# Kernel tuning notes

Measured on AMD Instinct MI355X. Metric: run time of the kernel, lower is better.

## Reference

```python
import jax, jax.numpy as jnp
import numpy as np

CH = 128
KSIZE = 7
BS, H, W = 8, 56, 56


def nbhd_extract(x, k):
    """Faithful replication of square_nbhd_extractor(k)(x) from the torch code,
    including its permute(0,2,1).reshape(bs,h,w,d) layout reinterpretation and
    the unfold over the last two dims of that layout. x: (bs, n, d) -> (bs, n, k*k, d)."""
    bs, n, d = x.shape
    h = w = int(np.sqrt(n))
    # torch: x.permute(0,2,1).reshape(bs,h,w,d)
    y = jnp.transpose(x, (0, 2, 1)).reshape(bs, h, w, d)
    # extract_image_patches treats y as (b, c=h, H=w, W=d); stride=1, dilation=1
    # pad both sliding dims by k-1 total ((k-1)//2 low, rest high)
    p_lo = (k - 1) // 2
    p_hi = (k - 1) - p_lo
    yp = jnp.pad(y, ((0, 0), (0, 0), (p_lo, p_hi), (p_lo, p_hi)))
    Hs, Ws = w, d  # output sliding sizes equal original dims (stride 1)
    # double unfold: window over dim2 at axis -2, window over dim3 at axis -1
    wins = jnp.stack([
        jnp.stack([yp[:, :, i:i + Hs, j:j + Ws] for j in range(k)], axis=-1)
        for i in range(k)], axis=-2)  # (bs, h, w, d, k, k)
    patches = jnp.transpose(wins, (0, 4, 5, 1, 2, 3))  # (bs, k, k, h, w, d)
    # torch: patches.view(bs, n, d, r).permute(0,1,3,2)
    return patches.reshape(bs, n, d, k * k).transpose(0, 1, 3, 2)  # (bs, n, r, d)


def setup_inputs() -> dict:
    key = jax.random.key(0)
    ks = jax.random.split(key, 3)
    x = jax.random.normal(ks[0], (BS, CH, H, W), dtype=jnp.float32)
    W1 = jax.random.normal(ks[1], (2, CH), dtype=jnp.float32) * np.float32(1.0 / np.sqrt(2.0))
    b1 = jnp.zeros((CH,), dtype=jnp.float32)
    W2 = jax.random.normal(ks[2], (CH, CH), dtype=jnp.float32) * np.float32(1.0 / np.sqrt(CH))
    b2 = jnp.zeros((CH,), dtype=jnp.float32)
    return {"x": x, "W1": W1, "b1": b1, "W2": W2, "b2": b2, "ksize": KSIZE}


def reference(x, W1, b1, W2, b2, ksize):
    bs, c, h, w = x.shape
    n = h * w
    # coords: meshgrid('ij') of linspace(-3,3), shape (1, n, 2)
    gi = jnp.linspace(-3.0, 3.0, h)
    gj = jnp.linspace(-3.0, 3.0, w)
    coords = jnp.stack(jnp.meshgrid(gi, gj, indexing='ij'), axis=-1).reshape(1, n, 2)
    rel = nbhd_extract(coords, ksize) - coords[:, :, None, :]  # (1, n, r, 2)
    # position MLP: Linear(2,ch) -> ReLU -> Linear(ch,ch)
    P = jax.nn.relu(rel @ W1 + b1) @ W2 + b2                   # (1, n, r, ch)
    Wsm = jax.nn.softmax(P, axis=2)[0]                          # (n, r, c) ; ch == c
    # values: gather neighborhood patches of channels-last points
    xp = jnp.transpose(x, (0, 2, 3, 1)).reshape(bs, n, c)
    V = nbhd_extract(xp, ksize)                                 # (bs, n, r, c)
    # head-folded weighting * value reduce over neighborhood == per-channel weighted sum
    out = jnp.einsum('nrc,bnrc->bnc', Wsm, V)                   # (bs, n, c)
    return jnp.transpose(out, (0, 2, 1)).reshape(bs, c, h, w)
```

## Files before the change

kernel.cpp:

```cpp
#include <hip/hip_runtime.h>

#define CH   128
#define KS   7
#define R    49
#define HH   56
#define NPOS 3136
#define BS   8
#define XSTR 401408
#define XTOT (BS*XSTR)

typedef short short8 __attribute__((ext_vector_type(8)));
typedef float f32x4  __attribute__((ext_vector_type(4)));
typedef unsigned int u32;
typedef unsigned long long u64;
typedef u32 u32x4 __attribute__((ext_vector_type(4)));

__device__ __forceinline__ short f2bf(float f) {
    unsigned u = __float_as_uint(f);
    u += 0x7fffu + ((u >> 16) & 1u);
    return (short)(u >> 16);
}
__device__ __forceinline__ float bf2f(short s) {
    return __uint_as_float(((unsigned)(unsigned short)s) << 16);
}
__device__ __forceinline__ float bf2f_u(u32 lo16) {
    return __uint_as_float(lo16 << 16);
}
__device__ __forceinline__ u64 bitrange(int a, int b) {
    a = a < 0 ? 0 : (a > 49 ? 49 : a);
    b = b < 0 ? 0 : (b > 49 ? 49 : b);
    if (b <= a) return 0ull;
    return (1ull << b) - (1ull << a);
}

#define HSTR 136
#define PSTR 132
#define NWIN 3140

__global__ __launch_bounds__(256) void poatt_prep(
    const float* __restrict__ W2, short* __restrict__ wsH, short* __restrict__ wsL)
{
    int t = blockIdx.x * 256 + threadIdx.x;
    int k = t >> 7, ch = t & 127;
    float w = W2[k * CH + ch];
    short hi = f2bf(w);
    wsH[ch * CH + k] = hi;
    wsL[ch * CH + k] = f2bf(w - bf2f(hi));
}

__global__ __launch_bounds__(256) void poatt_pc(
    const float* __restrict__ x, const float* __restrict__ W2,
    u32* __restrict__ x2, short* __restrict__ wsH, short* __restrict__ wsL)
{
    int t = blockIdx.x * 256 + threadIdx.x;
    const float4* xv = reinterpret_cast<const float4*>(x);
    float4 a = xv[2 * t], b = xv[2 * t + 1];
    u32x4 o;
    o[0] = (u32)(unsigned short)f2bf(a.x) | ((u32)(unsigned short)f2bf(a.y) << 16);
    o[1] = (u32)(unsigned short)f2bf(a.z) | ((u32)(unsigned short)f2bf(a.w) << 16);
    o[2] = (u32)(unsigned short)f2bf(b.x) | ((u32)(unsigned short)f2bf(b.y) << 16);
    o[3] = (u32)(unsigned short)f2bf(b.z) | ((u32)(unsigned short)f2bf(b.w) << 16);
    reinterpret_cast<u32x4*>(x2)[t] = o;

    if (t < CH * CH) {
        int k = t >> 7, ch = t & 127;
        float w = W2[k * CH + ch];
        short hi = f2bf(w);
        wsH[ch * CH + k] = hi;
        wsL[ch * CH + k] = f2bf(w - bf2f(hi));
    }
}

__global__ __launch_bounds__(256, 4) void poatt_fused(
    const u32* __restrict__ x2,
    const float* __restrict__ W1, const float* __restrict__ b1,
    const short* __restrict__ wsH, const short* __restrict__ wsL,
    float* __restrict__ trb)
{
    __shared__ float rel_s[R][2];
    __shared__ float part_s[CH];
    __shared__ u32 wpack[25 * CH];
    __shared__ __align__(16) char smem[64 * HSTR * 2];
    short* hid_s = (short*)smem;
    u32*   win   = (u32*)smem;

    const int pos = blockIdx.x;
    const int tid = threadIdx.x;
    const int ch  = tid & (CH - 1);
    const int g   = tid >> 7;

    const int q  = pos >> 6;
    const int s  = pos & 63;
    const int ii = q / KS;
    const int jj = q % KS;

    if (tid < 2 * R) {
        const int e  = (tid >= R) ? 1 : 0;
        const int rr = tid - e * R;
        int F  = (pos * 2 + e) * R + rr;
        int ep = F & 1;
        int t  = F >> 1;
        int jp = t % HH; t /= HH;
        int a  = t % HH; t /= HH;
        int jc = t % KS;
        int ic = t / KS;
        int row = jp + ic - 3;
        int col = ep + jc - 3;
        float v = 0.0f;
        if (row >= 0 && row < HH && (col == 0 || col == 1)) {
            int f    = a * (HH * 2) + row * 2 + col;
            int cidx = f / NPOS;
            int p    = f - cidx * NPOS;
            int u    = (cidx == 0) ? (p / HH) : (p % HH);
            v = -3.0f + 6.0f * (float)u * (1.0f / 55.0f);
        }
        const float c0 = -3.0f + 6.0f * (float)(pos / HH) * (1.0f / 55.0f);
        const float c1 = -3.0f + 6.0f * (float)(pos % HH) * (1.0f / 55.0f);
        rel_s[rr][e] = v - ((e == 0) ? c0 : c1);
    }
    __syncthreads();

    {
        const float w10 = W1[ch];
        const float w11 = W1[CH + ch];
        const float bb  = b1[ch];
        for (int rr = g; rr < R; rr += 2) {
            float h = fmaf(rel_s[rr][0], w10, fmaf(rel_s[rr][1], w11, bb));
            hid_s[rr * HSTR + ch] = f2bf(fmaxf(h, 0.0f));
        }
        for (int t = tid; t < 15 * HSTR; t += 256) hid_s[R * HSTR + t] = 0;
    }
    __syncthreads();

    const int winbase = s * (R * CH) + (ii - 3) * CH + (jj - 3);
    const int m2v = winbase & 1;
    const int hw  = winbase >> 1;
    const int m3  = hw & 3;
    const int cw0 = (hw - m3) >> 2;
    const u32x4* x2v = reinterpret_cast<const u32x4*>(x2);
    const unsigned short* x2s = reinterpret_cast<const unsigned short*>(x2);

    u32x4 v[4];
    auto ld = [&](int b) {
        const int cb = b * (XSTR >> 3) + cw0;
        const bool safe = (b > 0 || winbase >= 8) && (b < BS - 1 || winbase + 6280 <= XSTR);
        if (safe) {
            v[0] = x2v[cb + tid];
            v[1] = x2v[cb + tid + 256];
            v[2] = x2v[cb + tid + 512];
            if (tid < 17) v[3] = x2v[cb + tid + 768];
        } else {
            #pragma unroll
            for (int j = 0; j < 4; ++j) {
                if (j < 3 || tid < 17) {
                    int gc = cb + tid + 256 * j;
                    u32x4 o;
                    #pragma unroll
                    for (int kk = 0; kk < 4; ++kk) {
                        int e0 = 8 * gc + 2 * kk;
                        int a0 = e0;     a0 = a0 < 0 ? 0 : (a0 >= XTOT ? XTOT - 1 : a0);
                        int a1 = e0 + 1; a1 = a1 < 0 ? 0 : (a1 >= XTOT ? XTOT - 1 : a1);
                        o[kk] = (u32)x2s[a0] | ((u32)x2s[a1] << 16);
                    }
                    v[j] = o;
                }
            }
        }
    };
    auto st = [&]() {
        *reinterpret_cast<u32x4*>(&win[4 * tid])         = v[0];
        *reinterpret_cast<u32x4*>(&win[4 * (tid + 256)]) = v[1];
        *reinterpret_cast<u32x4*>(&win[4 * (tid + 512)]) = v[2];
        if (tid < 17)
            *reinterpret_cast<u32x4*>(&win[4 * (tid + 768)]) = v[3];
    };

    ld(0);

    const int wv_ = tid >> 6;
    const int l   = tid & 63;
    const int lr  = l & 15;
    const int kg  = l >> 4;

    f32x4 acc[4][2];
    #pragma unroll
    for (int mt = 0; mt < 4; ++mt) { acc[mt][0] = (f32x4)0.0f; acc[mt][1] = (f32x4)0.0f; }

    #pragma unroll
    for (int np = 0; np < 2; ++np) {
        const int bcol = 32 * wv_ + 16 * np + lr;
        short8 bH[4], bL[4];
        #pragma unroll
        for (int kk = 0; kk < 4; ++kk) {
            bH[kk] = *reinterpret_cast<const short8*>(wsH + bcol * CH + kk * 32 + kg * 8);
            bL[kk] = *reinterpret_cast<const short8*>(wsL + bcol * CH + kk * 32 + kg * 8);
        }
        #pragma unroll
        for (int mt = 0; mt < 4; ++mt) {
            #pragma unroll
            for (int kk = 0; kk < 4; ++kk) {
                short8 a = *reinterpret_cast<const short8*>(
                    &hid_s[(16 * mt + lr) * HSTR + kk * 32 + kg * 8]);
                acc[mt][np] = __builtin_amdgcn_mfma_f32_16x16x32_bf16(a, bH[kk], acc[mt][np], 0, 0, 0);
                acc[mt][np] = __builtin_amdgcn_mfma_f32_16x16x32_bf16(a, bL[kk], acc[mt][np], 0, 0, 0);
            }
        }
    }

    {
        float wv[4][4];
        #pragma unroll
        for (int np = 0; np < 2; ++np) {
            const int chh = 32 * wv_ + 16 * np + lr;

            float mx = -1e30f;
            #pragma unroll
            for (int mt = 0; mt < 4; ++mt)
                #pragma unroll
                for (int r = 0; r < 4; ++r) {
                    int rr = 16 * mt + 4 * kg + r;
                    if (rr < R) mx = fmaxf(mx, acc[mt][np][r]);
                }
            mx = fmaxf(mx, __shfl_xor(mx, 16));
            mx = fmaxf(mx, __shfl_xor(mx, 32));

            float sm = 0.0f;
            #pragma unroll
            for (int mt = 0; mt < 4; ++mt)
                #pragma unroll
                for (int r = 0; r < 4; ++r) {
                    int rr = 16 * mt + 4 * kg + r;
                    float e = (rr < R) ? __expf(acc[mt][np][r] - mx) : 0.0f;
                    wv[mt][r] = e;
                    sm += e;
                }
            sm += __shfl_xor(sm, 16);
            sm += __shfl_xor(sm, 32);
            const float inv = 1.0f / sm;

            const int base = s * (R * CH) + chh * R;
            const int e2_0 = base & 127;
            const int jb   = base >> 7;
            const int j2_0 = jb % HH;
            const int rw   = 128 - e2_0;
            int j2p = j2_0 + 1; if (j2p == HH) j2p = 0;
            const bool rok1 = (j2_0 >= 3 - ii) && (j2_0 < 59 - ii);
            const bool rok2 = (j2p  >= 3 - ii) && (j2p  < 59 - ii);
            const int c1 = (3 - jj) - e2_0;
            const int c2 = (131 - jj) - e2_0;
            const int lo2 = c2 < rw ? c2 : rw;
            const int hi2 = c2 < rw ? rw : c2;
            u64 colm = ~(bitrange(0, c1) | bitrange(lo2, hi2));
            u64 rowm = (rok1 ? bitrange(0, rw) : 0ull) | (rok2 ? bitrange(rw, 49) : 0ull);
            u64 vm = (colm & rowm) >> (kg << 2);
            const u32 vlo = (u32)vm, vhi = (u32)(vm >> 32);

            #pragma unroll
            for (int mt = 0; mt < 4; ++mt)
                #pragma unroll
                for (int r = 0; r < 4; ++r) {
                    int rr = 16 * mt + 4 * kg + r;
                    if (rr < R) {
                        const int bp = 16 * mt + r;
                        bool ok = (((bp < 32 ? vlo : vhi) >> (bp & 31)) & 1u) != 0;
                        wv[mt][r] = ok ? wv[mt][r] * inv : 0.0f;
                    }
                }

            #pragma unroll
            for (int mt = 0; mt < 4; ++mt)
                #pragma unroll
                for (int jp = 0; jp < 2; ++jp) {
                    int j = 8 * mt + 2 * kg + jp;
                    if (j <= 24) {
                        u32 pk = (u32)(unsigned short)f2bf(wv[mt][2 * jp])
                               | ((u32)(unsigned short)f2bf(wv[mt][2 * jp + 1]) << 16);
                        wpack[j * CH + chh] = pk;
                    }
                }
        }
    }
    __syncthreads();

    st();

    float qw[28];
    {
        const int j0 = g ? 13 : 0;
        const int nj = g ? 12 : 13;
        u32 wr[13];
        #pragma unroll
        for (int i = 0; i < 13; ++i) wr[i] = (i < nj) ? wpack[(j0 + i) * CH + ch] : 0u;
        float pw[26];
        #pragma unroll
        for (int i = 0; i < 13; ++i) {
            pw[2 * i]     = bf2f_u(wr[i] & 0xffffu);
            pw[2 * i + 1] = bf2f_u(wr[i] >> 16);
        }
        const int kw0 = g ? 26 : 0;
        const int par = (m2v + 49 * ch + kw0) & 1;
        #pragma unroll
        for (int k2 = 0; k2 < 28; ++k2) {
            float a_ = (k2 < 26) ? pw[k2] : 0.0f;
            float b_ = (k2 >= 1 && k2 <= 26) ? pw[k2 - 1] : 0.0f;
            qw[k2] = par ? b_ : a_;
        }
    }
    const int d0 = m3 + ((m2v + 49 * ch + (g ? 26 : 0)) >> 1);
    __syncthreads();

    for (int b = 0; b < BS; ++b) {
        if (b + 1 < BS) ld(b + 1);

        float acc2 = 0.0f;
        #pragma unroll
        for (int dd = 0; dd < 14; ++dd) {
            u32 wd = win[d0 + dd];
            acc2 = fmaf(__uint_as_float(wd << 16),         qw[2 * dd],     acc2);
            acc2 = fmaf(__uint_as_float(wd & 0xffff0000u), qw[2 * dd + 1], acc2);
        }
        if (g) part_s[ch] = acc2;
        __syncthreads();
        if (!g) trb[((size_t)b * NPOS + pos) * CH + ch] = acc2 + part_s[ch];
        if (b + 1 < BS) st();
        __syncthreads();
    }
}

__global__ __launch_bounds__(256) void poatt_tr(
    const float* __restrict__ ws, float* __restrict__ out)
{
    __shared__ float t[64 * 129];
    const int blk = blockIdx.x;
    const int b   = blk / 49;
    const int p0  = (blk % 49) * 64;
    const int tid = threadIdx.x;

    const int chR = tid & 127, pR = tid >> 7;
    #pragma unroll
    for (int r = 0; r < 32; ++r) {
        int pl = pR + 2 * r;
        t[pl * 129 + chR] = ws[((size_t)b * NPOS + p0 + pl) * CH + chR];
    }
    __syncthreads();
    const int pW = tid & 63, chW0 = tid >> 6;
    #pragma unroll
    for (int c = 0; c < 32; ++c) {
        int chl = chW0 + 4 * c;
        out[((size_t)b * CH + chl) * NPOS + p0 + pW] = t[pW * 129 + chl];
    }
}

template<bool WS_W2, bool USE_WS>
__global__ __launch_bounds__(256, 4) void poatt_mono(
    const float* __restrict__ x,
    const float* __restrict__ W1, const float* __restrict__ b1,
    const float* __restrict__ W2,
    const short* __restrict__ wsH, const short* __restrict__ wsL,
    float* __restrict__ dst)
{
    __shared__ float rel_s[R][2];
    __shared__ __align__(16) char smem[2 * 64 * HSTR * 2];
    short* hidH = (short*)smem;
    short* hidL = hidH + 64 * HSTR;
    float* Pbuf = (float*)smem;

    const int pos = blockIdx.x;
    const int tid = threadIdx.x;
    const int ch  = tid & (CH - 1);
    const int g   = tid >> 7;

    const int q  = pos >> 6;
    const int ii = q / KS;
    const int jj = q % KS;

    if (tid < 2 * R) {
        const int e  = (tid >= R) ? 1 : 0;
        const int rr = tid - e * R;
        int F  = (pos * 2 + e) * R + rr;
        int ep = F & 1;
        int t  = F >> 1;
        int jp = t % HH; t /= HH;
        int a  = t % HH; t /= HH;
        int jc = t % KS;
        int ic = t / KS;
        int row = jp + ic - 3;
        int col = ep + jc - 3;
        float v = 0.0f;
        if (row >= 0 && row < HH && (col == 0 || col == 1)) {
            int f    = a * (HH * 2) + row * 2 + col;
            int cidx = f / NPOS;
            int p    = f - cidx * NPOS;
            int u    = (cidx == 0) ? (p / HH) : (p % HH);
            v = -3.0f + 6.0f * (float)u * (1.0f / 55.0f);
        }
        const float c0 = -3.0f + 6.0f * (float)(pos / HH) * (1.0f / 55.0f);
        const float c1 = -3.0f + 6.0f * (float)(pos % HH) * (1.0f / 55.0f);
        rel_s[rr][e] = v - ((e == 0) ? c0 : c1);
    }
    __syncthreads();

    {
        const float w10 = W1[ch];
        const float w11 = W1[CH + ch];
        const float bb  = b1[ch];
        for (int rr = g; rr < R; rr += 2) {
            float h = fmaf(rel_s[rr][0], w10, fmaf(rel_s[rr][1], w11, bb));
            h = fmaxf(h, 0.0f);
            short hi = f2bf(h);
            hidH[rr * HSTR + ch] = hi;
            hidL[rr * HSTR + ch] = f2bf(h - bf2f(hi));
        }
        for (int t = tid; t < 15 * HSTR; t += 256) {
            hidH[R * HSTR + t] = 0;
            hidL[R * HSTR + t] = 0;
        }
    }
    __syncthreads();

    {
        const int w  = tid >> 6;
        const int l  = tid & 63;
        const int lr = l & 15;
        const int kg = l >> 4;

        short8 aH[4], aL[4];
        const int abase = (16 * w + lr) * HSTR + kg * 8;
        #pragma unroll
        for (int kk = 0; kk < 4; ++kk) {
            aH[kk] = *reinterpret_cast<const short8*>(&hidH[abase + kk * 32]);
            aL[kk] = *reinterpret_cast<const short8*>(&hidL[abase + kk * 32]);
        }

        f32x4 acc[8];
        #pragma unroll
        for (int n = 0; n < 8; ++n) acc[n] = (f32x4)0.0f;

        #pragma unroll
        for (int n = 0; n < 8; ++n) {
            const int bcol = 16 * n + lr;
            #pragma unroll
            for (int kk = 0; kk < 4; ++kk) {
                short8 bH, bL;
                if (WS_W2) {
                    bH = *reinterpret_cast<const short8*>(wsH + bcol * CH + kk * 32 + kg * 8);
                    bL = *reinterpret_cast<const short8*>(wsL + bcol * CH + kk * 32 + kg * 8);
                } else {
                    #pragma unroll
                    for (int j = 0; j < 8; ++j) {
                        float ww = ((const float*)W2)[(kk * 32 + kg * 8 + j) * CH + bcol];
                        short hi = f2bf(ww);
                        bH[j] = hi;
                        bL[j] = f2bf(ww - bf2f(hi));
                    }
                }
                acc[n] = __builtin_amdgcn_mfma_f32_16x16x32_bf16(aL[kk], bH, acc[n], 0, 0, 0);
                acc[n] = __builtin_amdgcn_mfma_f32_16x16x32_bf16(aH[kk], bL, acc[n], 0, 0, 0);
                acc[n] = __builtin_amdgcn_mfma_f32_16x16x32_bf16(aH[kk], bH, acc[n], 0, 0, 0);
            }
        }
        __syncthreads();

        #pragma unroll
        for (int n = 0; n < 8; ++n) {
            #pragma unroll
            for (int r = 0; r < 4; ++r) {
                int rr = 16 * w + kg * 4 + r;
                if (rr < R) Pbuf[rr * PSTR + 16 * n + lr] = acc[n][r];
            }
        }
    }
    __syncthreads();

    if (tid < CH) {
        float p[R];
        #pragma unroll
        for (int rr = 0; rr < R; ++rr) p[rr] = Pbuf[rr * PSTR + tid];
        float mx = p[0];
        #pragma unroll
        for (int rr = 1; rr < R; ++rr) mx = fmaxf(mx, p[rr]);
        float s = 0.0f;
        #pragma unroll
        for (int rr = 0; rr < R; ++rr) { p[rr] = __expf(p[rr] - mx); s += p[rr]; }
        const float inv = 1.0f / s;
        const int wb0 = (pos & 63) * (R * CH);
        #pragma unroll
        for (int rr = 0; rr < R; ++rr) {
            int rem = wb0 + tid * R + rr;
            int e2  = rem & (CH - 1);
            int j2  = (rem >> 7) % HH;
            int row = j2 + ii - 3;
            int col = e2 + jj - 3;
            bool valid = (row >= 0) && (row < HH) && (col >= 0) && (col < CH);
            Pbuf[rr * PSTR + tid] = valid ? p[rr] * inv : 0.0f;
        }
    }
    __syncthreads();

    float p[R];
    #pragma unroll
    for (int rr = 0; rr < R; ++rr) p[rr] = Pbuf[rr * PSTR + ch];

    const int winbase = (pos & 63) * (R * CH) + (ii - 3) * CH + (jj - 3);
    const int base_t  = winbase + ch * R;

    #pragma unroll
    for (int bi = 0; bi < 4; ++bi) {
        const int b  = g * 4 + bi;
        const int ab = b * XSTR + base_t;
        const bool safe = (b > 0 || winbase >= 0) && (b < BS - 1 || winbase + R * CH <= XSTR);
        float acc = 0.0f;
        if (safe) {
            #pragma unroll
            for (int rr = 0; rr < R; ++rr) acc = fmaf(p[rr], x[ab + rr], acc);
        } else {
            #pragma unroll
            for (int rr = 0; rr < R; ++rr) {
                int a2 = ab + rr;
                a2 = a2 < 0 ? 0 : (a2 >= XTOT ? XTOT - 1 : a2);
                acc = fmaf(p[rr], x[a2], acc);
            }
        }
        if (USE_WS) dst[((size_t)b * NPOS + pos) * CH + ch] = acc;
        else        dst[((size_t)b * CH + ch) * NPOS + pos] = acc;
    }
}

extern "C" void kernel_launch(void* const* d_in, const int* in_sizes, int n_in,
                              void* d_out, int out_size, void* d_ws, size_t ws_size,
                              hipStream_t stream) {
    (void)in_sizes; (void)n_in; (void)out_size;
    const float* x  = (const float*)d_in[0];
    const float* W1 = (const float*)d_in[1];
    const float* b1 = (const float*)d_in[2];
    const float* W2 = (const float*)d_in[3];
    float* out = (float*)d_out;

    const size_t W2T_BYTES = 2u * CH * CH * sizeof(short);
    const size_t X2_BYTES  = (size_t)XTOT * 2;
    const size_t TRB_BYTES = (size_t)BS * NPOS * CH * sizeof(float);
    const size_t FULL = W2T_BYTES + X2_BYTES + TRB_BYTES;

    short* wsH = (short*)d_ws;
    short* wsL = wsH + CH * CH;

    if (ws_size >= FULL) {
        u32*   x2  = (u32*)((char*)d_ws + W2T_BYTES);
        float* trb = (float*)((char*)d_ws + W2T_BYTES + X2_BYTES);

        poatt_pc<<<dim3(XTOT / (256 * 8)), dim3(256), 0, stream>>>(x, W2, x2, wsH, wsL);
        poatt_fused<<<dim3(NPOS), dim3(256), 0, stream>>>(x2, W1, b1, wsH, wsL, trb);
        poatt_tr<<<dim3(BS * 49), dim3(256), 0, stream>>>(trb, out);
    } else if (ws_size >= W2T_BYTES + TRB_BYTES) {
        float* trb = (float*)((char*)d_ws + W2T_BYTES);
        poatt_prep<<<dim3(64), dim3(256), 0, stream>>>(W2, wsH, wsL);
        poatt_mono<true, true><<<dim3(NPOS), dim3(256), 0, stream>>>(
            x, W1, b1, W2, wsH, wsL, trb);
        poatt_tr<<<dim3(BS * 49), dim3(256), 0, stream>>>(trb, out);
    } else if (ws_size >= W2T_BYTES) {
        poatt_prep<<<dim3(64), dim3(256), 0, stream>>>(W2, wsH, wsL);
        poatt_mono<true, false><<<dim3(NPOS), dim3(256), 0, stream>>>(
            x, W1, b1, W2, wsH, wsL, out);
    } else {
        poatt_mono<false, false><<<dim3(NPOS), dim3(256), 0, stream>>>(
            x, W1, b1, W2, nullptr, nullptr, out);
    }
}
```

Measured before the change: 75.53 us.

## Double-buffer batch window in LDS and reorder MFMA loop to reuse A fragments

The per-batch window load now goes into two ping-pong LDS buffers, reusing the wpack region as the second buffer. Prefetch runs two batches ahead, which removes one __syncthreads per batch iteration. The partial-sum buffer is also double-buffered so the single remaining barrier per batch is enough. Separately, the MFMA loop is reordered to load the A fragments once per k-slice and the B fragments per np, which changes register pressure and LDS traffic. Reusing wpack as a window buffer depends on qw having been fully read into registers before the first store, and on the 3136-word window fitting inside 25*128.

```diff
diff --git a/kernel.cpp b/kernel.cpp
--- a/kernel.cpp
+++ b/kernel.cpp
@@ -78,11 +78,12 @@
     float* __restrict__ trb)
 {
     __shared__ float rel_s[R][2];
-    __shared__ float part_s[CH];
+    __shared__ float part_s[2][CH];
     __shared__ u32 wpack[25 * CH];
     __shared__ __align__(16) char smem[64 * HSTR * 2];
     short* hid_s = (short*)smem;
-    u32*   win   = (u32*)smem;
+    u32*   win0  = (u32*)smem;
+    u32*   win1  = wpack;
 
     const int pos = blockIdx.x;
     const int tid = threadIdx.x;
@@ -167,12 +168,12 @@
             }
         }
     };
-    auto st = [&]() {
-        *reinterpret_cast<u32x4*>(&win[4 * tid])         = v[0];
-        *reinterpret_cast<u32x4*>(&win[4 * (tid + 256)]) = v[1];
-        *reinterpret_cast<u32x4*>(&win[4 * (tid + 512)]) = v[2];
+    auto st = [&](u32* wb) {
+        *reinterpret_cast<u32x4*>(&wb[4 * tid])         = v[0];
+        *reinterpret_cast<u32x4*>(&wb[4 * (tid + 256)]) = v[1];
+        *reinterpret_cast<u32x4*>(&wb[4 * (tid + 512)]) = v[2];
         if (tid < 17)
-            *reinterpret_cast<u32x4*>(&win[4 * (tid + 768)]) = v[3];
+            *reinterpret_cast<u32x4*>(&wb[4 * (tid + 768)]) = v[3];
     };
 
     ld(0);
@@ -187,22 +188,21 @@
     for (int mt = 0; mt < 4; ++mt) { acc[mt][0] = (f32x4)0.0f; acc[mt][1] = (f32x4)0.0f; }
 
     #pragma unroll
-    for (int np = 0; np < 2; ++np) {
-        const int bcol = 32 * wv_ + 16 * np + lr;
-        short8 bH[4], bL[4];
-        #pragma unroll
-        for (int kk = 0; kk < 4; ++kk) {
-            bH[kk] = *reinterpret_cast<const short8*>(wsH + bcol * CH + kk * 32 + kg * 8);
-            bL[kk] = *reinterpret_cast<const short8*>(wsL + bcol * CH + kk * 32 + kg * 8);
-        }
-        #pragma unroll
-        for (int mt = 0; mt < 4; ++mt) {
-            #pragma unroll
-            for (int kk = 0; kk < 4; ++kk) {
-                short8 a = *reinterpret_cast<const short8*>(
-                    &hid_s[(16 * mt + lr) * HSTR + kk * 32 + kg * 8]);
-                acc[mt][np] = __builtin_amdgcn_mfma_f32_16x16x32_bf16(a, bH[kk], acc[mt][np], 0, 0, 0);
-                acc[mt][np] = __builtin_amdgcn_mfma_f32_16x16x32_bf16(a, bL[kk], acc[mt][np], 0, 0, 0);
+    for (int kk = 0; kk < 4; ++kk) {
+        short8 aF[4];
+        #pragma unroll
+        for (int mt = 0; mt < 4; ++mt)
+            aF[mt] = *reinterpret_cast<const short8*>(
+                &hid_s[(16 * mt + lr) * HSTR + kk * 32 + kg * 8]);
+        #pragma unroll
+        for (int np = 0; np < 2; ++np) {
+            const int bcol = 32 * wv_ + 16 * np + lr;
+            short8 bH = *reinterpret_cast<const short8*>(wsH + bcol * CH + kk * 32 + kg * 8);
+            short8 bL = *reinterpret_cast<const short8*>(wsL + bcol * CH + kk * 32 + kg * 8);
+            #pragma unroll
+            for (int mt = 0; mt < 4; ++mt) {
+                acc[mt][np] = __builtin_amdgcn_mfma_f32_16x16x32_bf16(aF[mt], bH, acc[mt][np], 0, 0, 0);
+                acc[mt][np] = __builtin_amdgcn_mfma_f32_16x16x32_bf16(aF[mt], bL, acc[mt][np], 0, 0, 0);
             }
         }
     }
@@ -282,8 +282,6 @@
     }
     __syncthreads();
 
-    st();
-
     float qw[28];
     {
         const int j0 = g ? 13 : 0;
@@ -307,23 +305,29 @@
         }
     }
     const int d0 = m3 + ((m2v + 49 * ch + (g ? 26 : 0)) >> 1);
-    __syncthreads();
-
+
+    st(win0);
+    ld(1);
+    __syncthreads();
+
+    #pragma unroll
     for (int b = 0; b < BS; ++b) {
-        if (b + 1 < BS) ld(b + 1);
+        const u32* wb = (b & 1) ? win1 : win0;
 
         float acc2 = 0.0f;
         #pragma unroll
         for (int dd = 0; dd < 14; ++dd) {
-            u32 wd = win[d0 + dd];
+            u32 wd = wb[d0 + dd];
             acc2 = fmaf(__uint_as_float(wd << 16),         qw[2 * dd],     acc2);
             acc2 = fmaf(__uint_as_float(wd & 0xffff0000u), qw[2 * dd + 1], acc2);
         }
-        if (g) part_s[ch] = acc2;
+
+        if (b + 1 < BS) st((b & 1) ? win0 : win1);
+        if (b + 2 < BS) ld(b + 2);
+
+        if (g) part_s[b & 1][ch] = acc2;
         __syncthreads();
-        if (!g) trb[((size_t)b * NPOS + pos) * CH + ch] = acc2 + part_s[ch];
-        if (b + 1 < BS) st();
-        __syncthreads();
+        if (!g) trb[((size_t)b * NPOS + pos) * CH + ch] = acc2 + part_s[b & 1][ch];
     }
 }
 
```

After: 71.08 us. -5.9%, faster.
